# Performance work log

Hardware: AMD Instinct MI355X
Metric: run time of the kernel (lower is better)

Reference implementation:

```python
import jax, jax.numpy as jnp
import numpy as np

N_OBJ = 256   # number of RoIs/objects
C = 151       # num_obj_classes (Visual Genome)
H = 512       # hidden_dim == output_dim
T = 3         # time_step


def setup_inputs() -> dict:
    key = jax.random.key(0)
    ks = jax.random.split(key, 12)
    s = jnp.float32(0.02)

    def lin(k, out_dim, in_dim):
        k1, k2 = jax.random.split(k)
        w = jax.random.normal(k1, (out_dim, in_dim), jnp.float32) * s
        b = jax.random.normal(k2, (out_dim,), jnp.float32) * s
        return w, b

    inp = {}
    inp['input_ggnn'] = jax.random.normal(ks[0], (N_OBJ, H), jnp.float32)
    inp['matrix'] = jax.random.uniform(ks[1], (C, C), jnp.float32)
    for i, name in enumerate(['eq3_w', 'eq3_u', 'eq4_w', 'eq4_u', 'eq5_w', 'eq5_u']):
        in_dim = 2 * H if name.endswith('_w') else H
        w, b = lin(ks[2 + i], H, in_dim)
        inp['w_' + name] = w
        inp['b_' + name] = b
    w, b = lin(ks[8], H, 2 * H)
    inp['w_out'], inp['b_out'] = w, b
    w, b = lin(ks[9], C, C * H)
    inp['w_cls'], inp['b_cls'] = w, b
    return inp


def _ggnn_obj(input_ggnn, matrix,
              w_eq3_w, b_eq3_w, w_eq3_u, b_eq3_u,
              w_eq4_w, b_eq4_w, w_eq4_u, b_eq4_u,
              w_eq5_w, b_eq5_w, w_eq5_u, b_eq5_u,
              w_out, b_out, w_cls, b_cls):
    n = input_ggnn.shape[0]
    # hidden[i, c] = input_ggnn[i] for every class slot c  -> [N, C, H]
    hidden0 = jnp.broadcast_to(input_ggnn[:, None, :], (n, C, H))

    def step(hidden, _):
        hidden_sum = hidden.sum(axis=0)                # [C, H]
        x = hidden_sum[None, :, :] - hidden            # [N, C, H]
        # matrix.T @ x_i  and  matrix @ x_i, vectorized over N
        av1 = jnp.einsum('cd,nch->ndh', matrix, x)     # M^T propagation
        av2 = jnp.einsum('dc,nch->ndh', matrix, x)     # M propagation
        av = jnp.concatenate([av1, av2], axis=-1).reshape(n * C, 2 * H)
        h = hidden.reshape(n * C, H)
        zv = jax.nn.sigmoid(av @ w_eq3_w.T + b_eq3_w + h @ w_eq3_u.T + b_eq3_u)
        rv = jax.nn.sigmoid(av @ w_eq4_w.T + b_eq4_w + h @ w_eq4_u.T + b_eq4_u)
        hv = jnp.tanh(av @ w_eq5_w.T + b_eq5_w + (rv * h) @ w_eq5_u.T + b_eq5_u)
        h = (1.0 - zv) * h + zv * hv
        return h.reshape(n, C, H), None

    hidden, _ = jax.lax.scan(step, hidden0, None, length=T)

    inp_rep = hidden0.reshape(n * C, H)                # input repeated per class slot
    out = jnp.concatenate([hidden.reshape(n * C, H), inp_rep], axis=1)  # [N*C, 2H]
    out = jax.nn.relu(out @ w_out.T + b_out)           # [N*C, H]
    obj_dists = out.reshape(n, C * H) @ w_cls.T + b_cls  # [N, C]
    return obj_dists


def reference(input_ggnn, matrix,
              w_eq3_w, b_eq3_w, w_eq3_u, b_eq3_u,
              w_eq4_w, b_eq4_w, w_eq4_u, b_eq4_u,
              w_eq5_w, b_eq5_w, w_eq5_u, b_eq5_u,
              w_out, b_out, w_cls, b_cls):
    return _ggnn_obj(input_ggnn, matrix,
                     w_eq3_w, b_eq3_w, w_eq3_u, b_eq3_u,
                     w_eq4_w, b_eq4_w, w_eq4_u, b_eq4_u,
                     w_eq5_w, b_eq5_w, w_eq5_u, b_eq5_u,
                     w_out, b_out, w_cls, b_cls)
```

## Files before the change

kernel.cpp:

```cpp
#include <hip/hip_runtime.h>


#define C_     151
#define H_     512
#define NOBJ   256
#define NR     38656
#define NCH    64
#define CH     9664
#define CHP    9728
#define KPAD   160
#define KLDS   168
#define KA     2560
#define KV     3584
#define KB     2560

typedef _Float16 half8 __attribute__((ext_vector_type(8)));
typedef _Float16 half4 __attribute__((ext_vector_type(4)));
typedef float    f32x4 __attribute__((ext_vector_type(4)));

__device__ __forceinline__ float sigm(float x) { return 1.f / (1.f + expf(-x)); }

__device__ __forceinline__ void gload16(const void* g, void* l) {
    __builtin_amdgcn_global_load_lds(
        (const __attribute__((address_space(1))) void*)g,
        (__attribute__((address_space(3))) void*)l, 16, 0, 0);
}

__device__ __forceinline__ int kqswz(int s) {
    return 8 * (((s & 3) + 8 - ((s >> 2) & 3) - ((s >> 4) & 3)) & 3);
}
__device__ __forceinline__ int fraswz(int lane) {
    const int lb = lane & 15;
    return lb * 32 + 8 * (((lane >> 4) + lb + (lb >> 2)) & 3);
}

__device__ __forceinline__ half8 loadA8(const _Float16* p) { return *(const half8*)p; }
__device__ __forceinline__ half8 loadA8(const float* p) {
    f32x4 a = *(const f32x4*)p;
    f32x4 b = *(const f32x4*)(p + 4);
    half8 o;
    #pragma unroll
    for (int j = 0; j < 4; ++j) { o[j] = (_Float16)a[j]; o[4 + j] = (_Float16)b[j]; }
    return o;
}

template<int OP, typename AT, bool DUPK>
__global__ __launch_bounds__(256, 2)
void gemm_kernel(const AT* __restrict__ A, int lda,
                 const _Float16* __restrict__ B, int ldb,
                 void* __restrict__ Out, int ldo,
                 const float* __restrict__ bias,
                 const float* __restrict__ bias2,
                 int kchunk, int chunkStride)
{
    constexpr bool A16 = (sizeof(AT) == 2);
    __shared__ _Float16 sA[128 * 32];
    __shared__ _Float16 sB[128 * 32];
    const int tid  = threadIdx.x;
    const int lane = tid & 63;
    const int w    = tid >> 6;
    const int m0   = blockIdx.x * 128;
    const int n0   = blockIdx.y * 128;
    const int kbase = blockIdx.z * kchunk;

    const int s0 = tid, s1 = tid + 256;
    const AT* Ap0 = A + (size_t)(m0 + (s0 >> 2)) * lda + kqswz(s0);
    const AT* Ap1 = A + (size_t)(m0 + (s1 >> 2)) * lda + kqswz(s1);
    const _Float16* Bp0 = B + (size_t)(n0 + (s0 >> 2)) * ldb + kbase + kqswz(s0);
    const _Float16* Bp1 = B + (size_t)(n0 + (s1 >> 2)) * ldb + kbase + kqswz(s1);
    const int la0 = 8 * s0;
    const int la1 = 8 * s1;
    _Float16* lA0 = &sA[w * 512];
    _Float16* lA1 = &sA[2048 + w * 512];
    _Float16* lB0 = &sB[w * 512];
    _Float16* lB1 = &sB[2048 + w * 512];

    f32x4 acc[4][4];
    #pragma unroll
    for (int i = 0; i < 4; ++i)
        #pragma unroll
        for (int j = 0; j < 4; ++j)
            #pragma unroll
            for (int r = 0; r < 4; ++r) acc[i][j][r] = 0.f;

    const int mrow = (w >> 1) * 64;
    const int ncol = (w & 1) * 64;
    const int fra  = fraswz(lane);

    for (int k0 = 0; k0 < kchunk; k0 += 32) {
        int kA;
        if (DUPK) kA = (k0 < 2048) ? k0 : ((k0 < 3072) ? k0 - 2048 : k0 - 1024);
        else      kA = kbase + k0;
        if constexpr (A16) {
            __syncthreads();
            gload16(Ap0 + kA, lA0);
            gload16(Ap1 + kA, lA1);
            gload16(Bp0 + k0, lB0);
            gload16(Bp1 + k0, lB1);
            __syncthreads();
        } else {
            half8 va0 = loadA8(Ap0 + kA);
            half8 va1 = loadA8(Ap1 + kA);
            half8 vb0 = *(const half8*)(Bp0 + k0);
            half8 vb1 = *(const half8*)(Bp1 + k0);
            __syncthreads();
            *(half8*)&sA[la0] = va0;
            *(half8*)&sA[la1] = va1;
            *(half8*)&sB[la0] = vb0;
            *(half8*)&sB[la1] = vb1;
            __syncthreads();
        }
        half8 af[4], bf[4];
        #pragma unroll
        for (int i = 0; i < 4; ++i)
            af[i] = *(const half8*)&sA[(mrow + i * 16) * 32 + fra];
        #pragma unroll
        for (int i = 0; i < 4; ++i)
            bf[i] = *(const half8*)&sB[(ncol + i * 16) * 32 + fra];
        #pragma unroll
        for (int mi = 0; mi < 4; ++mi)
            #pragma unroll
            for (int ni = 0; ni < 4; ++ni)
                acc[mi][ni] = __builtin_amdgcn_mfma_f32_16x16x32_f16(af[mi], bf[ni], acc[mi][ni], 0, 0, 0);
    }

    const size_t zoff = (size_t)blockIdx.z * (size_t)chunkStride;
    #pragma unroll
    for (int mi = 0; mi < 4; ++mi) {
        #pragma unroll
        for (int ni = 0; ni < 4; ++ni) {
            #pragma unroll
            for (int r = 0; r < 4; ++r) {
                const int row = m0 + mrow + mi * 16 + (lane >> 4) * 4 + r;
                const int col = n0 + ncol + ni * 16 + (lane & 15);
                float v = acc[mi][ni][r];
                const size_t o = zoff + (size_t)row * ldo + col;
                if (OP == 0) {
                    ((float*)Out)[o] = v;
                } else if (OP == 1) {
                    ((_Float16*)Out)[o] = (_Float16)v;
                } else {
                    const unsigned n = (unsigned)row / 151u;
                    v += bias[col] + bias2[n * 512u + col];
                    v = v > 0.f ? v : 0.f;
                    ((_Float16*)Out)[o] = (_Float16)v;
                }
            }
        }
    }
}

template<int OP, bool DUPK>
__global__ __launch_bounds__(512, 2)
void gemm_wide(const _Float16* __restrict__ A, int lda,
               const _Float16* __restrict__ B, int ldb,
               void* __restrict__ Out, int ldo,
               int kchunk, int chunkStride)
{
    __shared__ _Float16 sA[2][128 * 32];
    __shared__ _Float16 sB[2][256 * 32];
    const int tid  = threadIdx.x;
    const int lane = tid & 63;
    const int w    = tid >> 6;
    const int m0   = blockIdx.x * 128;
    const int n0   = blockIdx.y * 256;
    const int kbase = blockIdx.z * kchunk;

    const int kq = kqswz(tid);
    const _Float16* Ap = A + (size_t)(m0 + (tid >> 2)) * lda + kq;
    const _Float16* Bp0 = B + (size_t)(n0 + (tid >> 2)) * ldb + kbase + kq;
    const _Float16* Bp1 = B + (size_t)(n0 + 128 + (tid >> 2)) * ldb + kbase + kq;
    _Float16* lA[2]  = { &sA[0][w * 512], &sA[1][w * 512] };
    _Float16* lB0[2] = { &sB[0][w * 512], &sB[1][w * 512] };
    _Float16* lB1[2] = { &sB[0][4096 + w * 512], &sB[1][4096 + w * 512] };

    f32x4 acc[4][4];
    #pragma unroll
    for (int i = 0; i < 4; ++i)
        #pragma unroll
        for (int j = 0; j < 4; ++j)
            #pragma unroll
            for (int r = 0; r < 4; ++r) acc[i][j][r] = 0.f;

    const int mrow = (w >> 2) * 64;
    const int ncol = (w & 3) * 64;
    const int fra  = fraswz(lane);

    for (int k0 = 0; k0 < kchunk; k0 += 64) {
        int kA[2], kB2[2];
        #pragma unroll
        for (int hf = 0; hf < 2; ++hf) {
            const int kk = k0 + 32 * hf;
            if (DUPK) {
                kA[hf]  = (kk < 2048) ? kk : ((kk < 3072) ? kk - 2048 : kk - 1024);
                kB2[hf] = (kk < 1024) ? kk : kk - 1024;
            } else {
                kA[hf]  = kbase + kk;
                kB2[hf] = kk;
            }
        }
        __syncthreads();
        #pragma unroll
        for (int hf = 0; hf < 2; ++hf) {
            gload16(Ap + kA[hf], lA[hf]);
            gload16(Bp0 + kB2[hf], lB0[hf]);
            gload16(Bp1 + kB2[hf], lB1[hf]);
        }
        __syncthreads();
        #pragma unroll
        for (int hf = 0; hf < 2; ++hf) {
            half8 af[4], bf[4];
            #pragma unroll
            for (int i = 0; i < 4; ++i)
                af[i] = *(const half8*)&sA[hf][(mrow + i * 16) * 32 + fra];
            #pragma unroll
            for (int i = 0; i < 4; ++i)
                bf[i] = *(const half8*)&sB[hf][(ncol + i * 16) * 32 + fra];
            #pragma unroll
            for (int mi = 0; mi < 4; ++mi)
                #pragma unroll
                for (int ni = 0; ni < 4; ++ni)
                    acc[mi][ni] = __builtin_amdgcn_mfma_f32_16x16x32_f16(af[mi], bf[ni], acc[mi][ni], 0, 0, 0);
        }
    }

    const size_t zoff = (size_t)blockIdx.z * (size_t)chunkStride;
    #pragma unroll
    for (int mi = 0; mi < 4; ++mi) {
        #pragma unroll
        for (int ni = 0; ni < 4; ++ni) {
            #pragma unroll
            for (int r = 0; r < 4; ++r) {
                const int row = m0 + mrow + mi * 16 + (lane >> 4) * 4 + r;
                const int col = n0 + ncol + ni * 16 + (lane & 15);
                const float v = acc[mi][ni][r];
                const size_t o = zoff + (size_t)row * ldo + col;
                if (OP == 0) ((float*)Out)[o] = v;
                else         ((_Float16*)Out)[o] = (_Float16)v;
            }
        }
    }
}

__global__ __launch_bounds__(256, 2)
void mix_kernel(const float* __restrict__ hid, const float* __restrict__ S,
                const _Float16* __restrict__ MTh, const _Float16* __restrict__ MTl,
                const _Float16* __restrict__ Mrh, const _Float16* __restrict__ Mrl,
                _Float16* __restrict__ AVH, int cbase)
{
    __shared__ _Float16 sxh[64 * KLDS];
    __shared__ _Float16 sxl[64 * KLDS];
    const int n  = blockIdx.x;
    const int h0 = blockIdx.y * 64;
    const int tid = threadIdx.x;

    #pragma unroll
    for (int i = 0; i < 5; ++i) {
        const int s  = tid + 256 * i;
        const int c  = s >> 3;
        const int hg = s & 7;
        half8 oh, ol;
        if (c < C_) {
            const float* hp = &hid[(size_t)(cbase + n * C_ + c) * H_ + h0 + hg * 8];
            const float* sp = &S[c * H_ + h0 + hg * 8];
            half8 hh;
            #pragma unroll
            for (int j = 0; j < 8; ++j) {
                const float hv = hp[j];
                const float x = sp[j] - hv;
                const _Float16 hi = (_Float16)x;
                oh[j] = hi;
                ol[j] = (_Float16)(x - (float)hi);
                hh[j] = (_Float16)hv;
            }
            *(half8*)&AVH[(size_t)(n * C_ + c) * KA + 2048 + h0 + hg * 8] = hh;
        } else {
            #pragma unroll
            for (int j = 0; j < 8; ++j) { oh[j] = (_Float16)0.f; ol[j] = (_Float16)0.f; }
        }
        #pragma unroll
        for (int j = 0; j < 8; ++j) {
            sxh[(hg * 8 + j) * KLDS + c] = oh[j];
            sxl[(hg * 8 + j) * KLDS + c] = ol[j];
        }
    }
    __syncthreads();

    const int lane = tid & 63;
    const int w    = tid >> 6;
    const _Float16* Mhi = (w >> 1) ? Mrh : MTh;
    const _Float16* Mlo = (w >> 1) ? Mrl : MTl;
    const int hb = (w & 1) * 32;

    f32x4 acc[10][2];
    #pragma unroll
    for (int i = 0; i < 10; ++i)
        #pragma unroll
        for (int j = 0; j < 2; ++j)
            #pragma unroll
            for (int r = 0; r < 4; ++r) acc[i][j][r] = 0.f;

    #pragma unroll
    for (int pass = 0; pass < 3; ++pass) {
        const _Float16* Ma = (pass == 2) ? Mlo : Mhi;
        const _Float16* X  = (pass == 1) ? sxl : sxh;
        #pragma unroll
        for (int kk = 0; kk < 5; ++kk) {
            const int k0 = kk * 32;
            half8 bf[2];
            #pragma unroll
            for (int ht = 0; ht < 2; ++ht)
                bf[ht] = *(const half8*)&X[(hb + ht * 16 + (lane & 15)) * KLDS + k0 + 8 * (lane >> 4)];
            #pragma unroll
            for (int dt = 0; dt < 10; ++dt) {
                half8 af = *(const half8*)&Ma[(dt * 16 + (lane & 15)) * KPAD + k0 + 8 * (lane >> 4)];
                acc[dt][0] = __builtin_amdgcn_mfma_f32_16x16x32_f16(af, bf[0], acc[dt][0], 0, 0, 0);
                acc[dt][1] = __builtin_amdgcn_mfma_f32_16x16x32_f16(af, bf[1], acc[dt][1], 0, 0, 0);
            }
        }
    }

    const int mixoff = (w >> 1) * 512;
    #pragma unroll
    for (int dt = 0; dt < 10; ++dt) {
        #pragma unroll
        for (int ht = 0; ht < 2; ++ht) {
            #pragma unroll
            for (int r = 0; r < 4; ++r) {
                const int d = dt * 16 + (lane >> 4) * 4 + r;
                if (d < C_) {
                    const int h = h0 + hb + ht * 16 + (lane & 15);
                    const float v = acc[dt][ht][r];
                    const _Float16 hi = (_Float16)v;
                    const _Float16 lo = (_Float16)(v - (float)hi);
                    _Float16* rowp = AVH + (size_t)(n * C_ + d) * KA + mixoff + h;
                    rowp[0]    = hi;
                    rowp[1024] = lo;
                }
            }
        }
    }
}


__global__ void k_sreduce(const float* __restrict__ hid, float* __restrict__ Stmp)
{
    const int c  = blockIdx.x;
    const int g  = blockIdx.y;
    const int hw = threadIdx.x;
    const float* p = hid + (size_t)c * H_ + hw * 8;
    float s[8];
    #pragma unroll
    for (int j = 0; j < 8; ++j) s[j] = 0.f;
    const size_t stride = (size_t)C_ * H_;
    for (int n = g * 32; n < g * 32 + 32; ++n) {
        f32x4 a = *(const f32x4*)(p + (size_t)n * stride);
        f32x4 b = *(const f32x4*)(p + (size_t)n * stride + 4);
        #pragma unroll
        for (int j = 0; j < 4; ++j) { s[j] += a[j]; s[4 + j] += b[j]; }
    }
    float* o = Stmp + (size_t)g * (C_ * H_) + c * H_ + hw * 8;
    *(f32x4*)o       = f32x4{s[0], s[1], s[2], s[3]};
    *(f32x4*)(o + 4) = f32x4{s[4], s[5], s[6], s[7]};
}

__global__ void k_sfold(const float* __restrict__ Stmp, float* __restrict__ S)
{
    const int idx = blockIdx.x * 256 + threadIdx.x;
    float s = 0.f;
    #pragma unroll
    for (int g = 0; g < 8; ++g) s += Stmp[(size_t)g * (C_ * H_) + idx];
    S[idx] = s;
}

__global__ void k_ew1(_Float16* __restrict__ pre, const float* __restrict__ hid,
                      const float* __restrict__ bz, const float* __restrict__ br, int cbase)
{
    const int idx = blockIdx.x * 256 + threadIdx.x;
    const unsigned r = idx >> 7;
    const int o4 = (idx & 127) << 2;
    const size_t base = (size_t)r * 1536;
    half4 zp = *(const half4*)&pre[base + o4];
    half4 rp = *(const half4*)&pre[base + 512 + o4];
    f32x4 hd = *(const f32x4*)&hid[(size_t)(cbase + r) * H_ + o4];
    f32x4 bz4 = *(const f32x4*)&bz[o4];
    f32x4 br4 = *(const f32x4*)&br[o4];
    half4 zs, rh;
    #pragma unroll
    for (int j = 0; j < 4; ++j) {
        float z = sigm((float)zp[j] + bz4[j]);
        float rr = sigm((float)rp[j] + br4[j]);
        zs[j] = (_Float16)z;
        rh[j] = (_Float16)(rr * hd[j]);
    }
    *(half4*)&pre[base + o4] = zs;
    *(half4*)&pre[base + 512 + o4] = rh;
}

__global__ void k_ew2(const _Float16* __restrict__ pre, const _Float16* __restrict__ p5a,
                      const _Float16* __restrict__ p5b,
                      float* __restrict__ hid, const float* __restrict__ b5, int cbase)
{
    const int idx = blockIdx.x * 256 + threadIdx.x;
    const unsigned r = idx >> 7;
    const int o4 = (idx & 127) << 2;
    const size_t base = (size_t)r * 1536;
    half4 w5 = *(const half4*)&pre[base + 1024 + o4];
    half4 pa = *(const half4*)&p5a[(size_t)r * H_ + o4];
    half4 pb = *(const half4*)&p5b[(size_t)r * H_ + o4];
    half4 zz = *(const half4*)&pre[base + o4];
    f32x4 hd = *(const f32x4*)&hid[(size_t)(cbase + r) * H_ + o4];
    f32x4 b54 = *(const f32x4*)&b5[o4];
    #pragma unroll
    for (int j = 0; j < 4; ++j) {
        float t = tanhf((float)w5[j] + (float)pa[j] + (float)pb[j] + b54[j]);
        float z = (float)zz[j];
        hd[j] = (1.f - z) * hd[j] + z * t;
    }
    *(f32x4*)&hid[(size_t)(cbase + r) * H_ + o4] = hd;
}


__global__ void prep_wbig(const float* w3w, const float* w3u,
                          const float* w4w, const float* w4u,
                          const float* w5w, const float* w5u,
                          _Float16* __restrict__ Wbig)
{
    const int idx = blockIdx.x * 256 + threadIdx.x;
    const int op = idx / KB;
    const int j = idx - op * KB;
    const int g = op >> 9, o = op & 511;
    const float* ww = (g == 0) ? w3w : (g == 1) ? w4w : w5w;
    const float* wu = (g == 0) ? w3u : (g == 1) ? w4u : w5u;
    _Float16 out;
    if (j < 1024) {
        out = (_Float16)ww[o * 1024 + j];
    } else if (j < 2048) {
        const float v = ww[o * 1024 + (j - 1024)];
        const _Float16 hi = (_Float16)v;
        out = (_Float16)(v - (float)hi);
    } else {
        out = (g < 2) ? (_Float16)wu[o * 512 + (j - 2048)] : (_Float16)0.f;
    }
    Wbig[idx] = out;
}

__global__ void prep_m(const float* __restrict__ matrix,
                       _Float16* __restrict__ MTh, _Float16* __restrict__ MTl,
                       _Float16* __restrict__ Mrh, _Float16* __restrict__ Mrl)
{
    const int idx = blockIdx.x * 256 + threadIdx.x;
    const int d = idx / KPAD, c = idx - d * KPAD;
    float vT = 0.f, vR = 0.f;
    if (d < C_ && c < C_) { vT = matrix[c * C_ + d]; vR = matrix[d * C_ + c]; }
    const _Float16 th = (_Float16)vT;
    const _Float16 rh = (_Float16)vR;
    MTh[idx] = th; MTl[idx] = (_Float16)(vT - (float)th);
    Mrh[idx] = rh; Mrl[idx] = (_Float16)(vR - (float)rh);
}

__global__ void prep_wout(const float* __restrict__ wout,
                          _Float16* __restrict__ WL, _Float16* __restrict__ WR)
{
    const int idx = blockIdx.x * 256 + threadIdx.x;
    const int o = idx >> 9, j = idx & 511;
    WL[idx] = (_Float16)wout[o * 1024 + j];
    WR[idx] = (_Float16)wout[o * 1024 + 512 + j];
}

__global__ void prep_wcls(const float* __restrict__ wcls, _Float16* __restrict__ w16)
{
    const int k = blockIdx.x * 256 + threadIdx.x;
    const int d = blockIdx.y;
    w16[(size_t)d * (C_ * H_) + k] = (_Float16)wcls[(size_t)d * (C_ * H_) + k];
}

__global__ void k_cast(const float* __restrict__ src, _Float16* __restrict__ dst, int n)
{
    const int i = blockIdx.x * 256 + threadIdx.x;
    if (i < n) dst[i] = (_Float16)src[i];
}

__global__ void prep_bias(const float* b3w, const float* b3u, const float* b4w,
                          const float* b4u, const float* b5w, const float* b5u,
                          float* bz, float* br, float* b5)
{
    const int i = threadIdx.x;
    bz[i] = b3w[i] + b3u[i];
    br[i] = b4w[i] + b4u[i];
    b5[i] = b5w[i] + b5u[i];
}

__global__ void prep_hid(const float* __restrict__ input, float* __restrict__ hid)
{
    const int idx = blockIdx.x * 256 + threadIdx.x;
    const unsigned row = idx >> 7;
    const int h4 = (idx & 127) << 2;
    const unsigned n = row / 151u;
    f32x4 v = *(const f32x4*)&input[(size_t)n * H_ + h4];
    *(f32x4*)&hid[(size_t)row * H_ + h4] = v;
}

__global__ void k_reduce(const float* __restrict__ partial, const float* __restrict__ bcls,
                         float* __restrict__ out)
{
    const int idx = blockIdx.x * 256 + threadIdx.x;
    const unsigned n = (unsigned)idx / 151u;
    const unsigned d = (unsigned)idx - n * 151u;
    float s = 0.f;
    for (int z = 0; z < C_; ++z)
        s += partial[(size_t)z * (NOBJ * 256) + n * 256 + d];
    out[idx] = s + bcls[d];
}


extern "C" void kernel_launch(void* const* d_in, const int* in_sizes, int n_in,
                              void* d_out, int out_size, void* d_ws, size_t ws_size,
                              hipStream_t stream)
{
    const float* input  = (const float*)d_in[0];
    const float* matrix = (const float*)d_in[1];
    const float* w3w = (const float*)d_in[2];
    const float* b3w = (const float*)d_in[3];
    const float* w3u = (const float*)d_in[4];
    const float* b3u = (const float*)d_in[5];
    const float* w4w = (const float*)d_in[6];
    const float* b4w = (const float*)d_in[7];
    const float* w4u = (const float*)d_in[8];
    const float* b4u = (const float*)d_in[9];
    const float* w5w = (const float*)d_in[10];
    const float* b5w = (const float*)d_in[11];
    const float* w5u = (const float*)d_in[12];
    const float* b5u = (const float*)d_in[13];
    const float* wout = (const float*)d_in[14];
    const float* bout = (const float*)d_in[15];
    const float* wcls = (const float*)d_in[16];
    const float* bcls = (const float*)d_in[17];
    float* obj = (float*)d_out;

    char* ws = (char*)d_ws;
    size_t off = 0;
    auto take = [&](size_t bytes) -> char* {
        off = (off + 255) & ~(size_t)255;
        char* p = ws + off;
        off += bytes;
        return p;
    };

    _Float16* Wbig  = (_Float16*)take((size_t)1536 * KB * 2);
    _Float16* MTh   = (_Float16*)take((size_t)KPAD * KPAD * 2);
    _Float16* MTl   = (_Float16*)take((size_t)KPAD * KPAD * 2);
    _Float16* Mrh   = (_Float16*)take((size_t)KPAD * KPAD * 2);
    _Float16* Mrl   = (_Float16*)take((size_t)KPAD * KPAD * 2);
    _Float16* W5u16 = (_Float16*)take((size_t)512 * 512 * 2);
    _Float16* WL16  = (_Float16*)take((size_t)512 * 512 * 2);
    _Float16* WR16  = (_Float16*)take((size_t)512 * 512 * 2);
    _Float16* in16  = (_Float16*)take((size_t)256 * 512 * 2);
    float*    bz    = (float*)take(512 * 4);
    float*    br    = (float*)take(512 * 4);
    float*    b5    = (float*)take(512 * 4);
    float*    Stmp  = (float*)take((size_t)8 * C_ * H_ * 4);
    float*    S32   = (float*)take((size_t)C_ * H_ * 4);
    float*    base  = (float*)take((size_t)256 * 512 * 4);
    float*    hid32 = (float*)take((size_t)NR * H_ * 4);
    _Float16* AVH   = (_Float16*)take((size_t)CHP * KA * 2);
    _Float16* prec  = (_Float16*)take((size_t)CHP * 1536 * 2);
    _Float16* p5u = AVH;
    _Float16* OUT16 = AVH;
    _Float16* Wcls16 = (_Float16*)hid32;
    float* partial = (float*)((char*)hid32 + (size_t)NOBJ * C_ * H_ * 2);

    (void)in_sizes; (void)n_in; (void)out_size; (void)ws_size;

    prep_wbig<<<dim3((1536 * KB) / 256), 256, 0, stream>>>(w3w, w3u, w4w, w4u, w5w, w5u, Wbig);
    prep_m<<<dim3((KPAD * KPAD) / 256), 256, 0, stream>>>(matrix, MTh, MTl, Mrh, Mrl);
    k_cast<<<dim3((512 * 512) / 256), 256, 0, stream>>>(w5u, W5u16, 512 * 512);
    prep_wout<<<dim3((512 * 512) / 256), 256, 0, stream>>>(wout, WL16, WR16);
    k_cast<<<dim3((256 * 512) / 256), 256, 0, stream>>>(input, in16, 256 * 512);
    prep_bias<<<dim3(1), 512, 0, stream>>>(b3w, b3u, b4w, b4u, b5w, b5u, bz, br, b5);
    prep_hid<<<dim3((NR * 128) / 256), 256, 0, stream>>>(input, hid32);
    gemm_kernel<0, _Float16, false><<<dim3(2, 4, 1), 256, 0, stream>>>(
        in16, 512, WR16, 512, base, 512, nullptr, nullptr, 512, 0);

    for (int t = 0; t < 3; ++t) {
        k_sreduce<<<dim3(C_, 8), 64, 0, stream>>>(hid32, Stmp);
        k_sfold<<<dim3((C_ * H_) / 256), 256, 0, stream>>>(Stmp, S32);
        for (int cc = 0; cc < 4; ++cc) {
            const int cbase = cc * CH;
            mix_kernel<<<dim3(NCH, 8), 256, 0, stream>>>(
                hid32, S32, MTh, MTl, Mrh, Mrl, AVH, cbase);
            gemm_wide<1, true><<<dim3(CHP / 128, 1536 / 256, 1), 512, 0, stream>>>(
                AVH, KA, Wbig, KB, prec, 1536, KV, 0);
            k_ew1<<<dim3((CH * 128) / 256), 256, 0, stream>>>(prec, hid32, bz, br, cbase);
            gemm_kernel<1, _Float16, false><<<dim3(CHP / 128, 4, 2), 256, 0, stream>>>(
                prec + 512, 1536, W5u16, 512, p5u, 512, nullptr, nullptr, 256, CHP * 512);
            k_ew2<<<dim3((CH * 128) / 256), 256, 0, stream>>>(
                prec, p5u, p5u + (size_t)CHP * 512, hid32, b5, cbase);
        }
    }

    gemm_kernel<2, float, false><<<dim3(NR / 128, 512 / 128, 1), 256, 0, stream>>>(
        hid32, 512, WL16, 512, OUT16, 512, bout, base, 512, 0);

    prep_wcls<<<dim3((C_ * H_) / 256, C_), 256, 0, stream>>>(wcls, Wcls16);
    gemm_kernel<0, _Float16, false><<<dim3(NOBJ / 128, 256 / 128, C_), 256, 0, stream>>>(
        OUT16, C_ * H_, Wcls16, C_ * H_, partial, 256, nullptr, nullptr, 512, NOBJ * 256);
    k_reduce<<<dim3(NR / 256), 256, 0, stream>>>(partial, bcls, obj);
}
```

Measured before the change: 2.582 ms.

## Replace wide GEMM with 256x256-tile double-buffered kernel using quadrant MFMA schedule

Replaces the 128x256-tile gate GEMM with a 256x256 tile that uses a 64-wide K step, an XOR-swizzled LDS layout and double-buffered global-to-LDS loads issued one iteration ahead. The MFMA work is split into four quadrants, with fragment loads interleaved between them and s_setprio raised during the MFMA bursts. The aim is more data reuse per byte loaded and overlap of memory traffic with compute. The cost is a 128 KB LDS footprint, a larger accumulator (more registers), and half as many blocks in the grid, which lowers occupancy and wave-level parallelism.

```diff
diff --git a/kernel.cpp b/kernel.cpp
--- a/kernel.cpp
+++ b/kernel.cpp
@@ -150,93 +150,136 @@
     }
 }
 
-template<int OP, bool DUPK>
 __global__ __launch_bounds__(512, 2)
-void gemm_wide(const _Float16* __restrict__ A, int lda,
-               const _Float16* __restrict__ B, int ldb,
-               void* __restrict__ Out, int ldo,
-               int kchunk, int chunkStride)
-{
-    __shared__ _Float16 sA[2][128 * 32];
-    __shared__ _Float16 sB[2][256 * 32];
+void gemm256(const _Float16* __restrict__ A, const _Float16* __restrict__ B,
+             _Float16* __restrict__ Out)
+{
+    constexpr int LDA = KA;
+    constexpr int LDB = KB;
+    constexpr int LDO = 1536;
+    constexpr int NT  = KV / 64;
+    __shared__ _Float16 lds[2][32768];
+
     const int tid  = threadIdx.x;
     const int lane = tid & 63;
     const int w    = tid >> 6;
-    const int m0   = blockIdx.x * 128;
+    const int m0   = blockIdx.x * 256;
     const int n0   = blockIdx.y * 256;
-    const int kbase = blockIdx.z * kchunk;
-
-    const int kq = kqswz(tid);
-    const _Float16* Ap = A + (size_t)(m0 + (tid >> 2)) * lda + kq;
-    const _Float16* Bp0 = B + (size_t)(n0 + (tid >> 2)) * ldb + kbase + kq;
-    const _Float16* Bp1 = B + (size_t)(n0 + 128 + (tid >> 2)) * ldb + kbase + kq;
-    _Float16* lA[2]  = { &sA[0][w * 512], &sA[1][w * 512] };
-    _Float16* lB0[2] = { &sB[0][w * 512], &sB[1][w * 512] };
-    _Float16* lB1[2] = { &sB[0][4096 + w * 512], &sB[1][4096 + w * 512] };
-
-    f32x4 acc[4][4];
-    #pragma unroll
-    for (int i = 0; i < 4; ++i)
+
+    const int tr  = tid >> 3;
+    const int swz = ((tid & 7) ^ (tr & 7)) << 3;
+    const _Float16* Ap = A + (size_t)(m0 + tr) * LDA + swz;
+    const _Float16* Bp = B + (size_t)(n0 + tr) * LDB + swz;
+    const int ldsbase = w << 9;
+
+    auto stage = [&](int buf, int kAb, int kBb) {
+        _Float16* L = &lds[buf][0];
+        #pragma unroll
+        for (int h = 0; h < 2; ++h) {
+            #pragma unroll
+            for (int r = 0; r < 2; ++r) {
+                const int ro = h * 128 + r * 64;
+                gload16(Ap + (size_t)ro * LDA + kAb, L + h * 8192 + r * 4096 + ldsbase);
+                gload16(Bp + (size_t)ro * LDB + kBb, L + 16384 + h * 8192 + r * 4096 + ldsbase);
+            }
+        }
+    };
+
+    const int lb = lane & 15;
+    const int lq = lane >> 4;
+    auto frag = [&](const _Float16* base, int row0, int ks) -> half8 {
+        const int row = row0 + lb;
+        const int kg  = ks * 4 + lq;
+        return *(const half8*)&base[row * 64 + ((kg ^ (row & 7)) << 3)];
+    };
+
+    const int wm = (w >> 2) * 128;
+    const int wn = (w & 3) * 64;
+
+    f32x4 acc[8][4];
+    #pragma unroll
+    for (int i = 0; i < 8; ++i)
         #pragma unroll
         for (int j = 0; j < 4; ++j)
             #pragma unroll
             for (int r = 0; r < 4; ++r) acc[i][j][r] = 0.f;
 
-    const int mrow = (w >> 2) * 64;
-    const int ncol = (w & 3) * 64;
-    const int fra  = fraswz(lane);
-
-    for (int k0 = 0; k0 < kchunk; k0 += 64) {
-        int kA[2], kB2[2];
-        #pragma unroll
-        for (int hf = 0; hf < 2; ++hf) {
-            const int kk = k0 + 32 * hf;
-            if (DUPK) {
-                kA[hf]  = (kk < 2048) ? kk : ((kk < 3072) ? kk - 2048 : kk - 1024);
-                kB2[hf] = (kk < 1024) ? kk : kk - 1024;
-            } else {
-                kA[hf]  = kbase + kk;
-                kB2[hf] = kk;
-            }
-        }
-        __syncthreads();
-        #pragma unroll
-        for (int hf = 0; hf < 2; ++hf) {
-            gload16(Ap + kA[hf], lA[hf]);
-            gload16(Bp0 + kB2[hf], lB0[hf]);
-            gload16(Bp1 + kB2[hf], lB1[hf]);
-        }
-        __syncthreads();
-        #pragma unroll
-        for (int hf = 0; hf < 2; ++hf) {
-            half8 af[4], bf[4];
-            #pragma unroll
-            for (int i = 0; i < 4; ++i)
-                af[i] = *(const half8*)&sA[hf][(mrow + i * 16) * 32 + fra];
-            #pragma unroll
-            for (int i = 0; i < 4; ++i)
-                bf[i] = *(const half8*)&sB[hf][(ncol + i * 16) * 32 + fra];
-            #pragma unroll
-            for (int mi = 0; mi < 4; ++mi)
-                #pragma unroll
-                for (int ni = 0; ni < 4; ++ni)
-                    acc[mi][ni] = __builtin_amdgcn_mfma_f32_16x16x32_f16(af[mi], bf[ni], acc[mi][ni], 0, 0, 0);
-        }
-    }
-
-    const size_t zoff = (size_t)blockIdx.z * (size_t)chunkStride;
-    #pragma unroll
-    for (int mi = 0; mi < 4; ++mi) {
+    half8 a[4][2], b0[2][2], b1[2][2];
+
+#define QUAD(MQ, NQ, BB) do {                                                   \
+    __builtin_amdgcn_s_barrier();                                               \
+    asm volatile("s_waitcnt lgkmcnt(0)" ::: "memory");                          \
+    __builtin_amdgcn_s_setprio(1);                                              \
+    _Pragma("unroll")                                                           \
+    for (int i = 0; i < 4; ++i) {                                               \
+        _Pragma("unroll")                                                       \
+        for (int j = 0; j < 2; ++j) {                                           \
+            _Pragma("unroll")                                                   \
+            for (int ks = 0; ks < 2; ++ks)                                      \
+                acc[(MQ) * 4 + i][(NQ) * 2 + j] =                               \
+                    __builtin_amdgcn_mfma_f32_16x16x32_f16(                     \
+                        a[i][ks], BB[j][ks],                                    \
+                        acc[(MQ) * 4 + i][(NQ) * 2 + j], 0, 0, 0);              \
+        }                                                                       \
+    }                                                                           \
+    __builtin_amdgcn_s_setprio(0);                                              \
+    __builtin_amdgcn_s_barrier();                                               \
+} while (0)
+
+    stage(0, 0, 0);
+    asm volatile("s_waitcnt vmcnt(0)" ::: "memory");
+    __builtin_amdgcn_s_barrier();
+
+    for (int t = 0; t < NT; ++t) {
+        const _Float16* sA = &lds[t & 1][0];
+        const _Float16* sB = &lds[t & 1][16384];
+
+        #pragma unroll
+        for (int i = 0; i < 4; ++i) {
+            a[i][0] = frag(sA, wm + i * 16, 0);
+            a[i][1] = frag(sA, wm + i * 16, 1);
+        }
+        #pragma unroll
+        for (int j = 0; j < 2; ++j) {
+            b0[j][0] = frag(sB, wn + j * 16, 0);
+            b0[j][1] = frag(sB, wn + j * 16, 1);
+        }
+        if (t + 1 < NT) {
+            const int kk  = (t + 1) * 64;
+            const int kAb = (kk < 2048) ? kk : ((kk < 3072) ? kk - 2048 : kk - 1024);
+            const int kBb = (kk < 1024) ? kk : kk - 1024;
+            stage((t + 1) & 1, kAb, kBb);
+        }
+        QUAD(0, 0, b0);
+
+        #pragma unroll
+        for (int j = 0; j < 2; ++j) {
+            b1[j][0] = frag(sB, wn + 32 + j * 16, 0);
+            b1[j][1] = frag(sB, wn + 32 + j * 16, 1);
+        }
+        QUAD(0, 1, b1);
+
+        #pragma unroll
+        for (int i = 0; i < 4; ++i) {
+            a[i][0] = frag(sA, wm + 64 + i * 16, 0);
+            a[i][1] = frag(sA, wm + 64 + i * 16, 1);
+        }
+        QUAD(1, 1, b1);
+
+        asm volatile("s_waitcnt vmcnt(0)" ::: "memory");
+        QUAD(1, 0, b0);
+    }
+#undef QUAD
+
+    #pragma unroll
+    for (int mi = 0; mi < 8; ++mi) {
         #pragma unroll
         for (int ni = 0; ni < 4; ++ni) {
             #pragma unroll
             for (int r = 0; r < 4; ++r) {
-                const int row = m0 + mrow + mi * 16 + (lane >> 4) * 4 + r;
-                const int col = n0 + ncol + ni * 16 + (lane & 15);
-                const float v = acc[mi][ni][r];
-                const size_t o = zoff + (size_t)row * ldo + col;
-                if (OP == 0) ((float*)Out)[o] = v;
-                else         ((_Float16*)Out)[o] = (_Float16)v;
+                const int row = m0 + wm + mi * 16 + (lane >> 4) * 4 + r;
+                const int col = n0 + wn + ni * 16 + (lane & 15);
+                Out[(size_t)row * LDO + col] = (_Float16)acc[mi][ni][r];
             }
         }
     }
@@ -589,8 +632,8 @@
             const int cbase = cc * CH;
             mix_kernel<<<dim3(NCH, 8), 256, 0, stream>>>(
                 hid32, S32, MTh, MTl, Mrh, Mrl, AVH, cbase);
-            gemm_wide<1, true><<<dim3(CHP / 128, 1536 / 256, 1), 512, 0, stream>>>(
-                AVH, KA, Wbig, KB, prec, 1536, KV, 0);
+            gemm256<<<dim3(CHP / 256, 1536 / 256, 1), 512, 0, stream>>>(
+                AVH, Wbig, prec);
             k_ew1<<<dim3((CH * 128) / 256), 256, 0, stream>>>(prec, hid32, bz, br, cbase);
             gemm_kernel<1, _Float16, false><<<dim3(CHP / 128, 4, 2), 256, 0, stream>>>(
                 prec + 512, 1536, W5u16, 512, p5u, 512, nullptr, nullptr, 256, CHP * 512);
```

Result: no change. 2.597 ms (+0.6%).
